# Kernel tuning notes

Hardware: AMD Instinct MI355X
Metric: run time of the kernel (lower is better)

The kernel has to match this reference:

```python
import jax, jax.numpy as jnp
import numpy as np

N_NODES = 100000
N_EDGES = 1600000
G_DIM, H1, H2 = 128, 64, 32
HEADS = 4
NUM_REL = 3
NUM_CLASSES = 7


def setup_inputs() -> dict:
    key = jax.random.key(0)
    ks = jax.random.split(key, 16)
    s = 0.05
    inp = {
        "x": jax.random.normal(ks[0], (N_NODES, G_DIM), dtype=jnp.float32),
        "lengths": N_NODES,
        "edge_index": jax.random.randint(ks[1], (2, N_EDGES), 0, N_NODES),
        "edge_type": jax.random.randint(ks[2], (N_EDGES,), 0, NUM_REL),
        # RGCNConv params (root weight + per-relation weights + bias)
        "W_rel": jax.random.normal(ks[3], (NUM_REL, G_DIM, H1), dtype=jnp.float32) * s,
        "W_root": jax.random.normal(ks[4], (G_DIM, H1), dtype=jnp.float32) * s,
        "b_rgcn": jax.random.normal(ks[5], (H1,), dtype=jnp.float32) * s,
        # TransformerConv params (heads*H2 = 128 output, concat=True default)
        "Wq": jax.random.normal(ks[6], (H1, HEADS * H2), dtype=jnp.float32) * s,
        "bq": jax.random.normal(ks[7], (HEADS * H2,), dtype=jnp.float32) * s,
        "Wk": jax.random.normal(ks[8], (H1, HEADS * H2), dtype=jnp.float32) * s,
        "bk": jax.random.normal(ks[9], (HEADS * H2,), dtype=jnp.float32) * s,
        "Wv": jax.random.normal(ks[10], (H1, HEADS * H2), dtype=jnp.float32) * s,
        "bv": jax.random.normal(ks[11], (HEADS * H2,), dtype=jnp.float32) * s,
        "Wskip": jax.random.normal(ks[12], (H1, HEADS * H2), dtype=jnp.float32) * s,
        "bskip": jax.random.normal(ks[13], (HEADS * H2,), dtype=jnp.float32) * s,
        # final classifier (in = heads*H2 since TransformerConv concat=True)
        "Wf": jax.random.normal(ks[14], (HEADS * H2, NUM_CLASSES), dtype=jnp.float32) * s,
        "bf": jax.random.normal(ks[15], (NUM_CLASSES,), dtype=jnp.float32) * s,
    }
    return inp


def _forward(x, edge_index, edge_type, W_rel, W_root, b_rgcn,
             Wq, bq, Wk, bk, Wv, bv, Wskip, bskip, Wf, bf):
    n = x.shape[0]
    src, dst = edge_index[0], edge_index[1]  # source -> target flow

    # ---- RGCNConv: root transform + per-relation mean aggregation ----
    h = x @ W_root + b_rgcn  # [N, H1]
    for r in range(NUM_REL):
        hr = x @ W_rel[r]  # [N, H1] transform at node level (cheap)
        mask = (edge_type == r)
        msg = jnp.where(mask[:, None], hr[src], 0.0)  # [E, H1]
        ssum = jax.ops.segment_sum(msg, dst, num_segments=n)
        cnt = jax.ops.segment_sum(mask.astype(x.dtype), dst, num_segments=n)
        h = h + jnp.where(cnt[:, None] > 0, ssum / jnp.maximum(cnt, 1.0)[:, None], 0.0)
    h = jax.nn.relu(h)

    # ---- TransformerConv (heads=4, concat=True, root skip) ----
    Q = (h @ Wq + bq).reshape(n, HEADS, H2)
    K = (h @ Wk + bk).reshape(n, HEADS, H2)
    V = (h @ Wv + bv).reshape(n, HEADS, H2)
    scores = jnp.sum(Q[dst] * K[src], axis=-1) / jnp.sqrt(jnp.asarray(H2, x.dtype))  # [E, HEADS]
    smax = jax.ops.segment_max(scores, dst, num_segments=n)  # [N, HEADS]
    e = jnp.exp(scores - smax[dst])
    denom = jax.ops.segment_sum(e, dst, num_segments=n)  # [N, HEADS]
    alpha = e / jnp.maximum(denom[dst], 1e-16)  # [E, HEADS]
    agg = jax.ops.segment_sum(alpha[..., None] * V[src], dst, num_segments=n)  # [N, HEADS, H2]
    out = agg.reshape(n, HEADS * H2) + h @ Wskip + bskip
    out = jax.nn.relu(out)

    return out @ Wf + bf  # [N, NUM_CLASSES]


def reference(x, lengths, edge_index, edge_type, W_rel, W_root, b_rgcn,
              Wq, bq, Wk, bk, Wv, bv, Wskip, bskip, Wf, bf):
    # lengths is accepted but unused by the original forward
    return _forward(x, edge_index, edge_type, W_rel, W_root, b_rgcn,
                    Wq, bq, Wk, bk, Wv, bv, Wskip, bskip, Wf, bf)
```

## Files before the change

### kernel.cpp

```cpp
#include <hip/hip_runtime.h>
#include <math.h>

#define N_NODES 100000
#define N_EDGES 1600000

typedef short short8 __attribute__((ext_vector_type(8)));
typedef float f32x4 __attribute__((ext_vector_type(4)));
typedef float f32x2 __attribute__((ext_vector_type(2)));
typedef _Float16 h2 __attribute__((ext_vector_type(2)));

#define QSC 0.25503540f

static __device__ __forceinline__ float bf2f(unsigned int u16) {
    return __uint_as_float(u16 << 16);
}
static __device__ __forceinline__ unsigned short f2bf(float f) {
    unsigned u = __float_as_uint(f);
    unsigned r = u + 0x7FFF + ((u >> 16) & 1);
    return (unsigned short)(r >> 16);
}
static __device__ __forceinline__ f32x2 bfpair(unsigned u) {
    f32x2 r;
    r.x = __uint_as_float(u << 16);
    r.y = __uint_as_float(u & 0xFFFF0000u);
    return r;
}
static __device__ __forceinline__ float dot8h(const h2* q, uint4 k) {
    h2 s = q[0] * __builtin_bit_cast(h2, k.x);
    s += q[1] * __builtin_bit_cast(h2, k.y);
    s += q[2] * __builtin_bit_cast(h2, k.z);
    s += q[3] * __builtin_bit_cast(h2, k.w);
    return (float)s.x + (float)s.y;
}
static __device__ __forceinline__ void pv8h(h2* o, float w, uint4 v) {
    _Float16 wh = (_Float16)w;
    o[0] += wh * __builtin_bit_cast(h2, v.x);
    o[1] += wh * __builtin_bit_cast(h2, v.y);
    o[2] += wh * __builtin_bit_cast(h2, v.z);
    o[3] += wh * __builtin_bit_cast(h2, v.w);
}

__global__ void repack_kernel(const float* __restrict__ Wrel, const float* __restrict__ Wroot,
                              const float* __restrict__ Wq, const float* __restrict__ Wk,
                              const float* __restrict__ Wv, const float* __restrict__ Wsk,
                              const float* __restrict__ bq, const float* __restrict__ bk,
                              const float* __restrict__ bv, const float* __restrict__ bsk,
                              unsigned short* __restrict__ W1t, unsigned short* __restrict__ W2t,
                              float* __restrict__ bcat) {
    int idx = blockIdx.x * 256 + threadIdx.x;
    if (idx < 128 * 256) {
        int k = idx >> 8, c = idx & 255;
        float v;
        if (c < 192) { int r = c >> 6, cc = c & 63; v = Wrel[r * 8192 + k * 64 + cc]; }
        else v = Wroot[k * 64 + (c - 192)];
        W1t[c * 128 + k] = f2bf(v);
    }
    int i2 = idx - 128 * 256;
    if (i2 >= 0 && i2 < 64 * 512) {
        int k = i2 >> 9, c = i2 & 511;
        float v;
        if (c < 128) v = Wq[k * 128 + c];
        else if (c < 256) v = Wk[k * 128 + c - 128];
        else if (c < 384) v = Wv[k * 128 + c - 256];
        else v = Wsk[k * 128 + c - 384];
        W2t[c * 64 + k] = f2bf(v);
    }
    int i3 = idx - 128 * 256 - 64 * 512;
    if (i3 >= 0 && i3 < 512) {
        float v;
        if (i3 < 128) v = bq[i3];
        else if (i3 < 256) v = bk[i3 - 128];
        else if (i3 < 384) v = bv[i3 - 256];
        else v = bsk[i3 - 384];
        bcat[i3] = v;
    }
}

__global__ void hist_kernel(const int* __restrict__ ei, const int* __restrict__ et,
                            int* __restrict__ cntr, int* __restrict__ rank) {
    int e = blockIdx.x * 256 + threadIdx.x;
    if (e < N_EDGES) rank[e] = atomicAdd(&cntr[et[e] * N_NODES + ei[N_EDGES + e]], 1);
}

__global__ void scanA_kernel(const int* __restrict__ cntr, int* __restrict__ part) {
    __shared__ int wsum[4];
    int t = threadIdx.x;
    int base = blockIdx.x * 1024 + t * 4;
    int s = 0;
    for (int i = 0; i < 4; i++) {
        int idx = base + i;
        if (idx < N_NODES) s += cntr[idx] + cntr[N_NODES + idx] + cntr[2 * N_NODES + idx];
    }
    for (int off = 1; off < 64; off <<= 1) s += __shfl_xor(s, off);
    if ((t & 63) == 0) wsum[t >> 6] = s;
    __syncthreads();
    if (t == 0) part[blockIdx.x] = wsum[0] + wsum[1] + wsum[2] + wsum[3];
}

__global__ void scanC_kernel(const int* __restrict__ cntr, const int* __restrict__ part,
                             uint4* __restrict__ bro) {
    __shared__ int wsum[4];
    __shared__ int ws2[4];
    int t = threadIdx.x;
    int lane = t & 63;
    int base = blockIdx.x * 1024 + t * 4;
    int c0v[4], c1v[4], c2v[4]; int tsum = 0;
    for (int i = 0; i < 4; i++) {
        int idx = base + i;
        if (idx < N_NODES) {
            c0v[i] = cntr[idx]; c1v[i] = cntr[N_NODES + idx]; c2v[i] = cntr[2 * N_NODES + idx];
        } else { c0v[i] = c1v[i] = c2v[i] = 0; }
        tsum += c0v[i] + c1v[i] + c2v[i];
    }
    int p = (t < blockIdx.x) ? part[t] : 0;
    for (int off = 1; off < 64; off <<= 1) p += __shfl_xor(p, off);
    if (lane == 0) ws2[t >> 6] = p;
    int x = tsum;
    for (int off = 1; off < 64; off <<= 1) { int y = __shfl_up(x, off); if (lane >= off) x += y; }
    if (lane == 63) wsum[t >> 6] = x;
    __syncthreads();
    if (t == 0) { int run = 0; for (int w = 0; w < 4; w++) { int tmp = wsum[w]; wsum[w] = run; run += tmp; } }
    __syncthreads();
    int bofs = ws2[0] + ws2[1] + ws2[2] + ws2[3];
    int excl = x - tsum + wsum[t >> 6] + bofs;
    for (int i = 0; i < 4; i++) {
        int idx = base + i;
        if (idx < N_NODES) {
            uint4 b;
            b.x = (unsigned)excl;
            b.y = (unsigned)(excl + c0v[i]);
            b.z = (unsigned)(excl + c0v[i] + c1v[i]);
            b.w = (unsigned)(excl + c0v[i] + c1v[i] + c2v[i]);
            bro[idx] = b;
        }
        excl += c0v[i] + c1v[i] + c2v[i];
    }
}

__global__ void scatter_kernel(const int* __restrict__ ei, const int* __restrict__ et,
                               const uint4* __restrict__ bro, const int* __restrict__ rank,
                               unsigned int* __restrict__ ep) {
    int e = blockIdx.x * 256 + threadIdx.x;
    if (e >= N_EDGES) return;
    int src = ei[e], dst = ei[N_EDGES + e], r = et[e], rk = rank[e];
    uint4 b = bro[dst];
    unsigned ofs = (r == 0) ? b.x : (r == 1) ? b.y : b.z;
    ep[ofs + rk] = ((unsigned)src << 2) | (unsigned)r;
}

__global__ __launch_bounds__(256) void gemm1_mfma(const float* __restrict__ X,
                                                  const unsigned short* __restrict__ W1t,
                                                  unsigned short* __restrict__ hr_all) {
    __shared__ unsigned short As[64][136];
    __shared__ unsigned short Bs[64][136];
    int t = threadIdx.x;
    int rb = blockIdx.x * 64;
    #pragma unroll
    for (int i = 0; i < 8; i++) {
        int lin = t + i * 256;
        int row = lin >> 5;
        int c4 = lin & 31;
        float4 v = make_float4(0.f, 0.f, 0.f, 0.f);
        int gr = rb + row;
        if (gr < N_NODES) v = *(const float4*)&X[gr * 128 + c4 * 4];
        unsigned w0 = (unsigned)f2bf(v.x) | ((unsigned)f2bf(v.y) << 16);
        unsigned w1 = (unsigned)f2bf(v.z) | ((unsigned)f2bf(v.w) << 16);
        *(uint2*)&As[row][c4 * 4] = make_uint2(w0, w1);
    }
    int w = t >> 6, l = t & 63;
    int wr = (w >> 1) * 32, wc = (w & 1) * 32;
    int lr = l & 15, lk = (l >> 4) * 8;
    int drow = (l >> 4) * 4;
    int dcol = l & 15;
    for (int cb4 = 0; cb4 < 4; cb4++) {
        int cb = cb4 * 64;
        __syncthreads();
        #pragma unroll
        for (int i = 0; i < 4; i++) {
            int lin = t + i * 256;
            int n = lin >> 4;
            int k8 = lin & 15;
            *(uint4*)&Bs[n][k8 * 8] = *(const uint4*)&W1t[(cb + n) * 128 + k8 * 8];
        }
        __syncthreads();
        f32x4 c00 = {0.f,0.f,0.f,0.f}, c01 = {0.f,0.f,0.f,0.f};
        f32x4 c10 = {0.f,0.f,0.f,0.f}, c11 = {0.f,0.f,0.f,0.f};
        #pragma unroll
        for (int kk = 0; kk < 128; kk += 32) {
            short8 a0 = *(const short8*)&As[wr + lr][kk + lk];
            short8 a1 = *(const short8*)&As[wr + 16 + lr][kk + lk];
            short8 b0 = *(const short8*)&Bs[wc + lr][kk + lk];
            short8 b1 = *(const short8*)&Bs[wc + 16 + lr][kk + lk];
            c00 = __builtin_amdgcn_mfma_f32_16x16x32_bf16(a0, b0, c00, 0, 0, 0);
            c01 = __builtin_amdgcn_mfma_f32_16x16x32_bf16(a0, b1, c01, 0, 0, 0);
            c10 = __builtin_amdgcn_mfma_f32_16x16x32_bf16(a1, b0, c10, 0, 0, 0);
            c11 = __builtin_amdgcn_mfma_f32_16x16x32_bf16(a1, b1, c11, 0, 0, 0);
        }
        f32x4 cc[2][2] = {{c00, c01}, {c10, c11}};
        #pragma unroll
        for (int i = 0; i < 2; i++)
            #pragma unroll
            for (int j = 0; j < 2; j++)
                #pragma unroll
                for (int rg = 0; rg < 4; rg++) {
                    int gr = rb + wr + i * 16 + drow + rg;
                    int gc = cb + wc + j * 16 + dcol;
                    if (gr < N_NODES) hr_all[gr * 256 + gc] = f2bf(cc[i][j][rg]);
                }
    }
}

__global__ __launch_bounds__(256) void rgcn_kernel(const unsigned short* __restrict__ hr,
                                                   const float* __restrict__ brg,
                                                   const uint4* __restrict__ bro,
                                                   const unsigned int* __restrict__ ep,
                                                   unsigned short* __restrict__ Hm) {
    int t = threadIdx.x, lane = t & 63;
    int n = blockIdx.x * 4 + (t >> 6);
    if (n >= N_NODES) return;
    int slot = lane >> 4, pos = lane & 15;
    const uint2* H2 = (const uint2*)hr;
    uint4 b = bro[n];
    int p0 = (int)b.x, p1 = (int)b.w;
    int c0 = (int)(b.y - b.x), c1 = (int)(b.z - b.y), c2 = (int)(b.w - b.z);
    float i0 = c0 ? 1.f / (float)c0 : 0.f;
    float i1 = c1 ? 1.f / (float)c1 : 0.f;
    float i2 = c2 ? 1.f / (float)c2 : 0.f;
    f32x2 a01 = {0.f, 0.f}, a23 = {0.f, 0.f};
    for (int base = p0; base < p1; base += 64) {
        int pc = base + lane;
        unsigned chunk = (pc < p1) ? ep[pc] : 0u;
        int cnt = min(64, p1 - base);
        int g0 = 0;
        for (; g0 + 16 <= cnt; g0 += 16) {
            int i0x = g0 + slot;
            int e0 = __shfl((int)chunk, i0x);
            int e1 = __shfl((int)chunk, i0x + 4);
            int e2 = __shfl((int)chunk, i0x + 8);
            int e3 = __shfl((int)chunk, i0x + 12);
            float w0 = ((e0 & 3) == 0) ? i0 : ((e0 & 3) == 1) ? i1 : i2;
            float w1 = ((e1 & 3) == 0) ? i0 : ((e1 & 3) == 1) ? i1 : i2;
            float w2 = ((e2 & 3) == 0) ? i0 : ((e2 & 3) == 1) ? i1 : i2;
            float w3 = ((e3 & 3) == 0) ? i0 : ((e3 & 3) == 1) ? i1 : i2;
            uint2 h0 = H2[(unsigned)e0 * 16 + pos];
            uint2 h1 = H2[(unsigned)e1 * 16 + pos];
            uint2 h2v = H2[(unsigned)e2 * 16 + pos];
            uint2 h3 = H2[(unsigned)e3 * 16 + pos];
            a01 += w0 * bfpair(h0.x); a23 += w0 * bfpair(h0.y);
            a01 += w1 * bfpair(h1.x); a23 += w1 * bfpair(h1.y);
            a01 += w2 * bfpair(h2v.x); a23 += w2 * bfpair(h2v.y);
            a01 += w3 * bfpair(h3.x); a23 += w3 * bfpair(h3.y);
        }
        for (; g0 < cnt; g0 += 8) {
            int iA = g0 + slot, iB = iA + 4;
            int e0 = __shfl((int)chunk, iA);
            int e1 = __shfl((int)chunk, iB);
            float w0 = ((e0 & 3) == 0) ? i0 : ((e0 & 3) == 1) ? i1 : i2;
            float w1 = ((e1 & 3) == 0) ? i0 : ((e1 & 3) == 1) ? i1 : i2;
            w0 = (iA < cnt) ? w0 : 0.f;
            w1 = (iB < cnt) ? w1 : 0.f;
            uint2 h0 = H2[(unsigned)e0 * 16 + pos];
            uint2 h1 = H2[(unsigned)e1 * 16 + pos];
            a01 += w0 * bfpair(h0.x); a23 += w0 * bfpair(h0.y);
            a01 += w1 * bfpair(h1.x); a23 += w1 * bfpair(h1.y);
        }
    }
    a01.x += __shfl_xor(a01.x, 16); a01.x += __shfl_xor(a01.x, 32);
    a01.y += __shfl_xor(a01.y, 16); a01.y += __shfl_xor(a01.y, 32);
    a23.x += __shfl_xor(a23.x, 16); a23.x += __shfl_xor(a23.x, 32);
    a23.y += __shfl_xor(a23.y, 16); a23.y += __shfl_xor(a23.y, 32);
    uint2 rt = H2[(n * 4 + 3) * 16 + pos];
    f32x2 r01 = bfpair(rt.x), r23 = bfpair(rt.y);
    float4 bb = ((const float4*)brg)[pos];
    float h0 = fmaxf(r01.x + bb.x + a01.x, 0.f);
    float h1 = fmaxf(r01.y + bb.y + a01.y, 0.f);
    float h2s = fmaxf(r23.x + bb.z + a23.x, 0.f);
    float h3 = fmaxf(r23.y + bb.w + a23.y, 0.f);
    if (slot == 0) {
        uint2 wv;
        wv.x = (unsigned)f2bf(h0) | ((unsigned)f2bf(h1) << 16);
        wv.y = (unsigned)f2bf(h2s) | ((unsigned)f2bf(h3) << 16);
        ((uint2*)Hm)[n * 16 + pos] = wv;
    }
}

__global__ __launch_bounds__(256) void gemm2_mfma(const unsigned short* __restrict__ Hm,
                                                  const unsigned short* __restrict__ W2t,
                                                  const float* __restrict__ bcat,
                                                  _Float16* __restrict__ QS, _Float16* __restrict__ KV) {
    __shared__ unsigned short As[64][72];
    __shared__ unsigned short Bs[64][72];
    int t = threadIdx.x;
    int rb = blockIdx.x * 64;
    #pragma unroll
    for (int i = 0; i < 2; i++) {
        int lin = t + i * 256;
        int row = lin >> 3;
        int k8 = lin & 7;
        uint4 v = make_uint4(0, 0, 0, 0);
        int gr = rb + row;
        if (gr < N_NODES) v = *(const uint4*)&Hm[gr * 64 + k8 * 8];
        *(uint4*)&As[row][k8 * 8] = v;
    }
    int w = t >> 6, l = t & 63;
    int wr = (w >> 1) * 32, wc = (w & 1) * 32;
    int lr = l & 15, lk = (l >> 4) * 8;
    int drow = (l >> 4) * 4;
    int dcol = l & 15;
    for (int cb8 = 0; cb8 < 8; cb8++) {
        int cb = cb8 * 64;
        float qsc = (cb8 < 2) ? QSC : 1.f;
        __syncthreads();
        #pragma unroll
        for (int i = 0; i < 2; i++) {
            int lin = t + i * 256;
            int n = lin >> 3;
            int k8 = lin & 7;
            *(uint4*)&Bs[n][k8 * 8] = *(const uint4*)&W2t[(cb + n) * 64 + k8 * 8];
        }
        __syncthreads();
        f32x4 c00 = {0.f,0.f,0.f,0.f}, c01 = {0.f,0.f,0.f,0.f};
        f32x4 c10 = {0.f,0.f,0.f,0.f}, c11 = {0.f,0.f,0.f,0.f};
        #pragma unroll
        for (int kk = 0; kk < 64; kk += 32) {
            short8 a0 = *(const short8*)&As[wr + lr][kk + lk];
            short8 a1 = *(const short8*)&As[wr + 16 + lr][kk + lk];
            short8 b0 = *(const short8*)&Bs[wc + lr][kk + lk];
            short8 b1 = *(const short8*)&Bs[wc + 16 + lr][kk + lk];
            c00 = __builtin_amdgcn_mfma_f32_16x16x32_bf16(a0, b0, c00, 0, 0, 0);
            c01 = __builtin_amdgcn_mfma_f32_16x16x32_bf16(a0, b1, c01, 0, 0, 0);
            c10 = __builtin_amdgcn_mfma_f32_16x16x32_bf16(a1, b0, c10, 0, 0, 0);
            c11 = __builtin_amdgcn_mfma_f32_16x16x32_bf16(a1, b1, c11, 0, 0, 0);
        }
        f32x4 cc[2][2] = {{c00, c01}, {c10, c11}};
        #pragma unroll
        for (int i = 0; i < 2; i++)
            #pragma unroll
            for (int j = 0; j < 2; j++)
                #pragma unroll
                for (int rg = 0; rg < 4; rg++) {
                    int gr = rb + wr + i * 16 + drow + rg;
                    int gc = cb + wc + j * 16 + dcol;
                    if (gr >= N_NODES) continue;
                    float v = (cc[i][j][rg] + bcat[gc]) * qsc;
                    _Float16 h = (_Float16)v;
                    if (gc < 128) QS[gr * 256 + gc] = h;
                    else if (gc < 384) KV[gr * 256 + gc - 128] = h;
                    else QS[gr * 256 + gc - 256] = h;
                }
    }
}

__global__ __launch_bounds__(256) void attn_kernel(const _Float16* __restrict__ QS,
                                                   const _Float16* __restrict__ KV,
                                                   const uint4* __restrict__ bro,
                                                   const unsigned int* __restrict__ ep,
                                                   const float* __restrict__ Wf, const float* __restrict__ bfv,
                                                   float* __restrict__ out) {
    int t = threadIdx.x, lane = t & 63;
    int n = blockIdx.x * 4 + (t >> 6);
    if (n >= N_NODES) return;
    int slot = lane >> 4, pos = lane & 15;
    const uint4* KV4 = (const uint4*)KV;
    const uint4* QS4 = (const uint4*)QS;
    uint4 qv = QS4[n * 32 + pos];
    h2 qh[4] = { __builtin_bit_cast(h2, qv.x), __builtin_bit_cast(h2, qv.y),
                 __builtin_bit_cast(h2, qv.z), __builtin_bit_cast(h2, qv.w) };
    h2 o[4] = { h2{0,0}, h2{0,0}, h2{0,0}, h2{0,0} };
    float d = 0.f;
    uint4 bnd = bro[n];
    int p0 = (int)bnd.x, p1 = (int)bnd.w;
    for (int base = p0; base < p1; base += 64) {
        int pc = base + lane;
        unsigned chunk = (pc < p1) ? ep[pc] : 0u;
        int cnt = min(64, p1 - base);
        int g0 = 0;
        for (; g0 + 16 <= cnt; g0 += 16) {
            int i0 = g0 + slot;
            int e0 = __shfl((int)chunk, i0);
            int e1 = __shfl((int)chunk, i0 + 4);
            int e2 = __shfl((int)chunk, i0 + 8);
            int e3 = __shfl((int)chunk, i0 + 12);
            int b0 = ((e0 >> 2) << 5) + pos;
            int b1 = ((e1 >> 2) << 5) + pos;
            int b2 = ((e2 >> 2) << 5) + pos;
            int b3 = ((e3 >> 2) << 5) + pos;
            uint4 k0 = KV4[b0], v0 = KV4[b0 + 16];
            uint4 k1 = KV4[b1], v1 = KV4[b1 + 16];
            uint4 k2 = KV4[b2], v2 = KV4[b2 + 16];
            uint4 k3 = KV4[b3], v3 = KV4[b3 + 16];
            float d0 = dot8h(qh, k0);
            float d1 = dot8h(qh, k1);
            float d2 = dot8h(qh, k2);
            float d3 = dot8h(qh, k3);
            d0 += __shfl_xor(d0, 1); d1 += __shfl_xor(d1, 1); d2 += __shfl_xor(d2, 1); d3 += __shfl_xor(d3, 1);
            d0 += __shfl_xor(d0, 2); d1 += __shfl_xor(d1, 2); d2 += __shfl_xor(d2, 2); d3 += __shfl_xor(d3, 2);
            float w0 = __builtin_amdgcn_exp2f(d0);
            float w1 = __builtin_amdgcn_exp2f(d1);
            float w2 = __builtin_amdgcn_exp2f(d2);
            float w3 = __builtin_amdgcn_exp2f(d3);
            d += (w0 + w1) + (w2 + w3);
            pv8h(o, w0, v0); pv8h(o, w1, v1); pv8h(o, w2, v2); pv8h(o, w3, v3);
        }
        for (; g0 < cnt; g0 += 8) {
            int iA = g0 + slot, iB = iA + 4;
            int e0 = __shfl((int)chunk, iA);
            int e1 = __shfl((int)chunk, iB);
            int b0 = ((e0 >> 2) << 5) + pos;
            int b1 = ((e1 >> 2) << 5) + pos;
            uint4 k0 = KV4[b0], v0 = KV4[b0 + 16];
            uint4 k1 = KV4[b1], v1 = KV4[b1 + 16];
            float d0 = dot8h(qh, k0);
            float d1 = dot8h(qh, k1);
            d0 += __shfl_xor(d0, 1); d1 += __shfl_xor(d1, 1);
            d0 += __shfl_xor(d0, 2); d1 += __shfl_xor(d1, 2);
            float w0 = (iA < cnt) ? __builtin_amdgcn_exp2f(d0) : 0.f;
            float w1 = (iB < cnt) ? __builtin_amdgcn_exp2f(d1) : 0.f;
            d += w0 + w1;
            pv8h(o, w0, v0); pv8h(o, w1, v1);
        }
    }
    float of[8];
    #pragma unroll
    for (int i = 0; i < 4; i++) { of[2 * i] = (float)o[i].x; of[2 * i + 1] = (float)o[i].y; }
    d += __shfl_xor(d, 16); d += __shfl_xor(d, 32);
    #pragma unroll
    for (int i = 0; i < 8; i++) { of[i] += __shfl_xor(of[i], 16); of[i] += __shfl_xor(of[i], 32); }
    float inv = (d > 0.f) ? 1.f / d : 0.f;
    uint4 sv = QS4[n * 32 + 16 + pos];
    h2 sh[4] = { __builtin_bit_cast(h2, sv.x), __builtin_bit_cast(h2, sv.y),
                 __builtin_bit_cast(h2, sv.z), __builtin_bit_cast(h2, sv.w) };
    float rf[8];
    #pragma unroll
    for (int i = 0; i < 4; i++) {
        rf[2 * i]     = fmaxf((float)sh[i].x + of[2 * i] * inv, 0.f);
        rf[2 * i + 1] = fmaxf((float)sh[i].y + of[2 * i + 1] * inv, 0.f);
    }
    float rr0 = (slot == 0) ? rf[0] : (slot == 1) ? rf[2] : (slot == 2) ? rf[4] : rf[6];
    float rr1 = (slot == 0) ? rf[1] : (slot == 1) ? rf[3] : (slot == 2) ? rf[5] : rf[7];
    int gd = pos * 8 + slot * 2;
    float acc[7];
    #pragma unroll
    for (int j = 0; j < 7; j++) acc[j] = rr0 * Wf[gd * 7 + j] + rr1 * Wf[gd * 7 + 7 + j];
    #pragma unroll
    for (int j = 0; j < 7; j++) {
        acc[j] += __shfl_xor(acc[j], 1);
        acc[j] += __shfl_xor(acc[j], 2);
        acc[j] += __shfl_xor(acc[j], 4);
        acc[j] += __shfl_xor(acc[j], 8);
        acc[j] += __shfl_xor(acc[j], 16);
        acc[j] += __shfl_xor(acc[j], 32);
    }
    if (lane == 0) {
        #pragma unroll
        for (int j = 0; j < 7; j++) out[n * 7 + j] = acc[j] + bfv[j];
    }
}

extern "C" void kernel_launch(void* const* d_in, const int* in_sizes, int n_in,
                              void* d_out, int out_size, void* d_ws, size_t ws_size,
                              hipStream_t stream) {
    const float* x     = (const float*)d_in[0];
    const int*   ei    = (const int*)d_in[2];
    const int*   et    = (const int*)d_in[3];
    const float* Wrel  = (const float*)d_in[4];
    const float* Wroot = (const float*)d_in[5];
    const float* brg   = (const float*)d_in[6];
    const float* Wq    = (const float*)d_in[7];
    const float* bq    = (const float*)d_in[8];
    const float* Wk    = (const float*)d_in[9];
    const float* bk    = (const float*)d_in[10];
    const float* Wv    = (const float*)d_in[11];
    const float* bv    = (const float*)d_in[12];
    const float* Wsk   = (const float*)d_in[13];
    const float* bsk   = (const float*)d_in[14];
    const float* Wf    = (const float*)d_in[15];
    const float* bfv   = (const float*)d_in[16];
    float* out = (float*)d_out;

    char* ws = (char*)d_ws;
    unsigned short* hr_all = (unsigned short*)(ws + 0);
    _Float16*       QS     = (_Float16*)(ws + 0);
    _Float16*       KV     = (_Float16*)(ws + 51200000);
    unsigned short* Hm     = (unsigned short*)(ws + 102400000);
    unsigned int*   ep     = (unsigned int*)(ws + 115200000);
    int*            rank   = (int*)(ws + 121600000);
    uint4*          bro    = (uint4*)(ws + 128000000);
    int*            cntr   = (int*)(ws + 129600016);
    int*            part   = (int*)(ws + 130800016);
    unsigned short* W1t    = (unsigned short*)(ws + 130800528);
    unsigned short* W2t    = (unsigned short*)(ws + 130866064);
    float*          bcat   = (float*)(ws + 130931600);

    hipMemsetAsync(cntr, 0, 3 * N_NODES * sizeof(int), stream);

    repack_kernel<<<258, 256, 0, stream>>>(Wrel, Wroot, Wq, Wk, Wv, Wsk, bq, bk, bv, bsk, W1t, W2t, bcat);

    hist_kernel<<<N_EDGES / 256, 256, 0, stream>>>(ei, et, cntr, rank);
    scanA_kernel<<<98, 256, 0, stream>>>(cntr, part);
    scanC_kernel<<<98, 256, 0, stream>>>(cntr, part, bro);
    scatter_kernel<<<N_EDGES / 256, 256, 0, stream>>>(ei, et, bro, rank, ep);

    gemm1_mfma<<<1563, 256, 0, stream>>>(x, W1t, hr_all);
    rgcn_kernel<<<25000, 256, 0, stream>>>(hr_all, brg, bro, ep, Hm);

    gemm2_mfma<<<1563, 256, 0, stream>>>(Hm, W2t, bcat, QS, KV);
    attn_kernel<<<25000, 256, 0, stream>>>(QS, KV, bro, ep, Wf, bfv, out);
}
```

Baseline: 440.1 us.

## Store K/V in FP8, simplify edge loops, pack relation into rank

K and V are stored as FP8 (when the conversion builtins exist), halving the gather traffic in the attention kernel, and accumulation moves to fp32. The shuffle-based chunked edge loops in the RGCN and attention kernels become direct per-slot ep loads. The relation type is packed into the rank word so the scatter kernel skips reading edge_type. The classifier epilogue is also restructured to use fewer shuffles. FP8 K/V lowers accuracy and may exceed tolerance.

```diff
diff --git a/kernel.cpp b/kernel.cpp
--- a/kernel.cpp
+++ b/kernel.cpp
@@ -10,6 +10,15 @@
 typedef _Float16 h2 __attribute__((ext_vector_type(2)));
 
 #define QSC 0.25503540f
+
+#if defined(__has_builtin)
+#if __has_builtin(__builtin_amdgcn_cvt_pk_f32_fp8) && __has_builtin(__builtin_amdgcn_cvt_pk_fp8_f32)
+#define HAVE_FP8 1
+#endif
+#endif
+#ifndef HAVE_FP8
+#define HAVE_FP8 0
+#endif
 
 static __device__ __forceinline__ float bf2f(unsigned int u16) {
     return __uint_as_float(u16 << 16);
@@ -24,20 +33,6 @@
     r.x = __uint_as_float(u << 16);
     r.y = __uint_as_float(u & 0xFFFF0000u);
     return r;
-}
-static __device__ __forceinline__ float dot8h(const h2* q, uint4 k) {
-    h2 s = q[0] * __builtin_bit_cast(h2, k.x);
-    s += q[1] * __builtin_bit_cast(h2, k.y);
-    s += q[2] * __builtin_bit_cast(h2, k.z);
-    s += q[3] * __builtin_bit_cast(h2, k.w);
-    return (float)s.x + (float)s.y;
-}
-static __device__ __forceinline__ void pv8h(h2* o, float w, uint4 v) {
-    _Float16 wh = (_Float16)w;
-    o[0] += wh * __builtin_bit_cast(h2, v.x);
-    o[1] += wh * __builtin_bit_cast(h2, v.y);
-    o[2] += wh * __builtin_bit_cast(h2, v.z);
-    o[3] += wh * __builtin_bit_cast(h2, v.w);
 }
 
 __global__ void repack_kernel(const float* __restrict__ Wrel, const float* __restrict__ Wroot,
@@ -77,9 +72,13 @@
 }
 
 __global__ void hist_kernel(const int* __restrict__ ei, const int* __restrict__ et,
-                            int* __restrict__ cntr, int* __restrict__ rank) {
+                            int* __restrict__ cntr, unsigned* __restrict__ rank) {
     int e = blockIdx.x * 256 + threadIdx.x;
-    if (e < N_EDGES) rank[e] = atomicAdd(&cntr[et[e] * N_NODES + ei[N_EDGES + e]], 1);
+    if (e < N_EDGES) {
+        int r = et[e];
+        unsigned rk = (unsigned)atomicAdd(&cntr[r * N_NODES + ei[N_EDGES + e]], 1);
+        rank[e] = rk | ((unsigned)r << 28);
+    }
 }
 
 __global__ void scanA_kernel(const int* __restrict__ cntr, int* __restrict__ part) {
@@ -137,12 +136,15 @@
     }
 }
 
-__global__ void scatter_kernel(const int* __restrict__ ei, const int* __restrict__ et,
-                               const uint4* __restrict__ bro, const int* __restrict__ rank,
+__global__ void scatter_kernel(const int* __restrict__ ei,
+                               const uint4* __restrict__ bro, const unsigned* __restrict__ rank,
                                unsigned int* __restrict__ ep) {
     int e = blockIdx.x * 256 + threadIdx.x;
     if (e >= N_EDGES) return;
-    int src = ei[e], dst = ei[N_EDGES + e], r = et[e], rk = rank[e];
+    int src = ei[e], dst = ei[N_EDGES + e];
+    unsigned rkr = rank[e];
+    int r = (int)(rkr >> 28);
+    unsigned rk = rkr & 0x0FFFFFFFu;
     uint4 b = bro[dst];
     unsigned ofs = (r == 0) ? b.x : (r == 1) ? b.y : b.z;
     ep[ofs + rk] = ((unsigned)src << 2) | (unsigned)r;
@@ -227,43 +229,29 @@
     float i1 = c1 ? 1.f / (float)c1 : 0.f;
     float i2 = c2 ? 1.f / (float)c2 : 0.f;
     f32x2 a01 = {0.f, 0.f}, a23 = {0.f, 0.f};
-    for (int base = p0; base < p1; base += 64) {
-        int pc = base + lane;
-        unsigned chunk = (pc < p1) ? ep[pc] : 0u;
-        int cnt = min(64, p1 - base);
-        int g0 = 0;
-        for (; g0 + 16 <= cnt; g0 += 16) {
-            int i0x = g0 + slot;
-            int e0 = __shfl((int)chunk, i0x);
-            int e1 = __shfl((int)chunk, i0x + 4);
-            int e2 = __shfl((int)chunk, i0x + 8);
-            int e3 = __shfl((int)chunk, i0x + 12);
-            float w0 = ((e0 & 3) == 0) ? i0 : ((e0 & 3) == 1) ? i1 : i2;
-            float w1 = ((e1 & 3) == 0) ? i0 : ((e1 & 3) == 1) ? i1 : i2;
-            float w2 = ((e2 & 3) == 0) ? i0 : ((e2 & 3) == 1) ? i1 : i2;
-            float w3 = ((e3 & 3) == 0) ? i0 : ((e3 & 3) == 1) ? i1 : i2;
-            uint2 h0 = H2[(unsigned)e0 * 16 + pos];
-            uint2 h1 = H2[(unsigned)e1 * 16 + pos];
-            uint2 h2v = H2[(unsigned)e2 * 16 + pos];
-            uint2 h3 = H2[(unsigned)e3 * 16 + pos];
-            a01 += w0 * bfpair(h0.x); a23 += w0 * bfpair(h0.y);
-            a01 += w1 * bfpair(h1.x); a23 += w1 * bfpair(h1.y);
-            a01 += w2 * bfpair(h2v.x); a23 += w2 * bfpair(h2v.y);
-            a01 += w3 * bfpair(h3.x); a23 += w3 * bfpair(h3.y);
-        }
-        for (; g0 < cnt; g0 += 8) {
-            int iA = g0 + slot, iB = iA + 4;
-            int e0 = __shfl((int)chunk, iA);
-            int e1 = __shfl((int)chunk, iB);
-            float w0 = ((e0 & 3) == 0) ? i0 : ((e0 & 3) == 1) ? i1 : i2;
-            float w1 = ((e1 & 3) == 0) ? i0 : ((e1 & 3) == 1) ? i1 : i2;
-            w0 = (iA < cnt) ? w0 : 0.f;
-            w1 = (iB < cnt) ? w1 : 0.f;
-            uint2 h0 = H2[(unsigned)e0 * 16 + pos];
-            uint2 h1 = H2[(unsigned)e1 * 16 + pos];
-            a01 += w0 * bfpair(h0.x); a23 += w0 * bfpair(h0.y);
-            a01 += w1 * bfpair(h1.x); a23 += w1 * bfpair(h1.y);
-        }
+    int idx = p0 + slot;
+    while (idx + 12 < p1) {
+        unsigned e0 = ep[idx], e1 = ep[idx + 4], e2 = ep[idx + 8], e3 = ep[idx + 12];
+        uint2 h0 = H2[e0 * 16 + pos];
+        uint2 h1 = H2[e1 * 16 + pos];
+        uint2 h2v = H2[e2 * 16 + pos];
+        uint2 h3 = H2[e3 * 16 + pos];
+        float w0 = ((e0 & 3) == 0) ? i0 : ((e0 & 3) == 1) ? i1 : i2;
+        float w1 = ((e1 & 3) == 0) ? i0 : ((e1 & 3) == 1) ? i1 : i2;
+        float w2 = ((e2 & 3) == 0) ? i0 : ((e2 & 3) == 1) ? i1 : i2;
+        float w3 = ((e3 & 3) == 0) ? i0 : ((e3 & 3) == 1) ? i1 : i2;
+        a01 += w0 * bfpair(h0.x); a23 += w0 * bfpair(h0.y);
+        a01 += w1 * bfpair(h1.x); a23 += w1 * bfpair(h1.y);
+        a01 += w2 * bfpair(h2v.x); a23 += w2 * bfpair(h2v.y);
+        a01 += w3 * bfpair(h3.x); a23 += w3 * bfpair(h3.y);
+        idx += 16;
+    }
+    while (idx < p1) {
+        unsigned e0 = ep[idx];
+        uint2 h0 = H2[e0 * 16 + pos];
+        float w0 = ((e0 & 3) == 0) ? i0 : ((e0 & 3) == 1) ? i1 : i2;
+        a01 += w0 * bfpair(h0.x); a23 += w0 * bfpair(h0.y);
+        idx += 4;
     }
     a01.x += __shfl_xor(a01.x, 16); a01.x += __shfl_xor(a01.x, 32);
     a01.y += __shfl_xor(a01.y, 16); a01.y += __shfl_xor(a01.y, 32);
@@ -287,7 +275,12 @@
 __global__ __launch_bounds__(256) void gemm2_mfma(const unsigned short* __restrict__ Hm,
                                                   const unsigned short* __restrict__ W2t,
                                                   const float* __restrict__ bcat,
-                                                  _Float16* __restrict__ QS, _Float16* __restrict__ KV) {
+                                                  _Float16* __restrict__ QS, void* __restrict__ KVp) {
+#if HAVE_FP8
+    unsigned char* KV = (unsigned char*)KVp;
+#else
+    _Float16* KV = (_Float16*)KVp;
+#endif
     __shared__ unsigned short As[64][72];
     __shared__ unsigned short Bs[64][72];
     int t = threadIdx.x;
@@ -343,16 +336,63 @@
                     int gc = cb + wc + j * 16 + dcol;
                     if (gr >= N_NODES) continue;
                     float v = (cc[i][j][rg] + bcat[gc]) * qsc;
-                    _Float16 h = (_Float16)v;
-                    if (gc < 128) QS[gr * 256 + gc] = h;
-                    else if (gc < 384) KV[gr * 256 + gc - 128] = h;
-                    else QS[gr * 256 + gc - 256] = h;
+                    if (gc < 128) QS[gr * 256 + gc] = (_Float16)v;
+                    else if (gc < 384) {
+#if HAVE_FP8
+                        unsigned pk = (unsigned)__builtin_amdgcn_cvt_pk_fp8_f32(v, v, 0, false);
+                        KV[gr * 256 + gc - 128] = (unsigned char)(pk & 0xFF);
+#else
+                        KV[gr * 256 + gc - 128] = (_Float16)v;
+#endif
+                    }
+                    else QS[gr * 256 + gc - 256] = (_Float16)v;
                 }
     }
 }
 
+#if HAVE_FP8
+static __device__ __forceinline__ void attn_edge(const f32x2* qf, uint2 ku, uint2 vu,
+                                                 f32x2& o01, f32x2& o23, f32x2& o45, f32x2& o67,
+                                                 float& d) {
+    f32x2 k01 = __builtin_amdgcn_cvt_pk_f32_fp8(ku.x, false);
+    f32x2 k23 = __builtin_amdgcn_cvt_pk_f32_fp8(ku.x, true);
+    f32x2 k45 = __builtin_amdgcn_cvt_pk_f32_fp8(ku.y, false);
+    f32x2 k67 = __builtin_amdgcn_cvt_pk_f32_fp8(ku.y, true);
+    f32x2 s2 = qf[0] * k01 + qf[1] * k23 + qf[2] * k45 + qf[3] * k67;
+    float s = s2.x + s2.y;
+    s += __shfl_xor(s, 1);
+    s += __shfl_xor(s, 2);
+    float w = __builtin_amdgcn_exp2f(s);
+    d += w;
+    o01 += w * __builtin_amdgcn_cvt_pk_f32_fp8(vu.x, false);
+    o23 += w * __builtin_amdgcn_cvt_pk_f32_fp8(vu.x, true);
+    o45 += w * __builtin_amdgcn_cvt_pk_f32_fp8(vu.y, false);
+    o67 += w * __builtin_amdgcn_cvt_pk_f32_fp8(vu.y, true);
+}
+#else
+static __device__ __forceinline__ void attn_edge16(const f32x2* qf, uint4 ku, uint4 vu,
+                                                   f32x2& o01, f32x2& o23, f32x2& o45, f32x2& o67,
+                                                   float& d) {
+    h2 k0 = __builtin_bit_cast(h2, ku.x), k1 = __builtin_bit_cast(h2, ku.y);
+    h2 k2 = __builtin_bit_cast(h2, ku.z), k3 = __builtin_bit_cast(h2, ku.w);
+    f32x2 s2 = qf[0] * f32x2{(float)k0.x, (float)k0.y} + qf[1] * f32x2{(float)k1.x, (float)k1.y}
+             + qf[2] * f32x2{(float)k2.x, (float)k2.y} + qf[3] * f32x2{(float)k3.x, (float)k3.y};
+    float s = s2.x + s2.y;
+    s += __shfl_xor(s, 1);
+    s += __shfl_xor(s, 2);
+    float w = __builtin_amdgcn_exp2f(s);
+    d += w;
+    h2 v0 = __builtin_bit_cast(h2, vu.x), v1 = __builtin_bit_cast(h2, vu.y);
+    h2 v2 = __builtin_bit_cast(h2, vu.z), v3 = __builtin_bit_cast(h2, vu.w);
+    o01 += w * f32x2{(float)v0.x, (float)v0.y};
+    o23 += w * f32x2{(float)v1.x, (float)v1.y};
+    o45 += w * f32x2{(float)v2.x, (float)v2.y};
+    o67 += w * f32x2{(float)v3.x, (float)v3.y};
+}
+#endif
+
 __global__ __launch_bounds__(256) void attn_kernel(const _Float16* __restrict__ QS,
-                                                   const _Float16* __restrict__ KV,
+                                                   const void* __restrict__ KVp,
                                                    const uint4* __restrict__ bro,
                                                    const unsigned int* __restrict__ ep,
                                                    const float* __restrict__ Wf, const float* __restrict__ bfv,
@@ -361,99 +401,96 @@
     int n = blockIdx.x * 4 + (t >> 6);
     if (n >= N_NODES) return;
     int slot = lane >> 4, pos = lane & 15;
-    const uint4* KV4 = (const uint4*)KV;
     const uint4* QS4 = (const uint4*)QS;
     uint4 qv = QS4[n * 32 + pos];
-    h2 qh[4] = { __builtin_bit_cast(h2, qv.x), __builtin_bit_cast(h2, qv.y),
-                 __builtin_bit_cast(h2, qv.z), __builtin_bit_cast(h2, qv.w) };
-    h2 o[4] = { h2{0,0}, h2{0,0}, h2{0,0}, h2{0,0} };
+    h2 q0 = __builtin_bit_cast(h2, qv.x), q1 = __builtin_bit_cast(h2, qv.y);
+    h2 q2 = __builtin_bit_cast(h2, qv.z), q3 = __builtin_bit_cast(h2, qv.w);
+    f32x2 qf[4] = { f32x2{(float)q0.x, (float)q0.y}, f32x2{(float)q1.x, (float)q1.y},
+                    f32x2{(float)q2.x, (float)q2.y}, f32x2{(float)q3.x, (float)q3.y} };
+    f32x2 o01 = {0.f,0.f}, o23 = {0.f,0.f}, o45 = {0.f,0.f}, o67 = {0.f,0.f};
     float d = 0.f;
     uint4 bnd = bro[n];
     int p0 = (int)bnd.x, p1 = (int)bnd.w;
-    for (int base = p0; base < p1; base += 64) {
-        int pc = base + lane;
-        unsigned chunk = (pc < p1) ? ep[pc] : 0u;
-        int cnt = min(64, p1 - base);
-        int g0 = 0;
-        for (; g0 + 16 <= cnt; g0 += 16) {
-            int i0 = g0 + slot;
-            int e0 = __shfl((int)chunk, i0);
-            int e1 = __shfl((int)chunk, i0 + 4);
-            int e2 = __shfl((int)chunk, i0 + 8);
-            int e3 = __shfl((int)chunk, i0 + 12);
-            int b0 = ((e0 >> 2) << 5) + pos;
-            int b1 = ((e1 >> 2) << 5) + pos;
-            int b2 = ((e2 >> 2) << 5) + pos;
-            int b3 = ((e3 >> 2) << 5) + pos;
-            uint4 k0 = KV4[b0], v0 = KV4[b0 + 16];
-            uint4 k1 = KV4[b1], v1 = KV4[b1 + 16];
-            uint4 k2 = KV4[b2], v2 = KV4[b2 + 16];
-            uint4 k3 = KV4[b3], v3 = KV4[b3 + 16];
-            float d0 = dot8h(qh, k0);
-            float d1 = dot8h(qh, k1);
-            float d2 = dot8h(qh, k2);
-            float d3 = dot8h(qh, k3);
-            d0 += __shfl_xor(d0, 1); d1 += __shfl_xor(d1, 1); d2 += __shfl_xor(d2, 1); d3 += __shfl_xor(d3, 1);
-            d0 += __shfl_xor(d0, 2); d1 += __shfl_xor(d1, 2); d2 += __shfl_xor(d2, 2); d3 += __shfl_xor(d3, 2);
-            float w0 = __builtin_amdgcn_exp2f(d0);
-            float w1 = __builtin_amdgcn_exp2f(d1);
-            float w2 = __builtin_amdgcn_exp2f(d2);
-            float w3 = __builtin_amdgcn_exp2f(d3);
-            d += (w0 + w1) + (w2 + w3);
-            pv8h(o, w0, v0); pv8h(o, w1, v1); pv8h(o, w2, v2); pv8h(o, w3, v3);
-        }
-        for (; g0 < cnt; g0 += 8) {
-            int iA = g0 + slot, iB = iA + 4;
-            int e0 = __shfl((int)chunk, iA);
-            int e1 = __shfl((int)chunk, iB);
-            int b0 = ((e0 >> 2) << 5) + pos;
-            int b1 = ((e1 >> 2) << 5) + pos;
-            uint4 k0 = KV4[b0], v0 = KV4[b0 + 16];
-            uint4 k1 = KV4[b1], v1 = KV4[b1 + 16];
-            float d0 = dot8h(qh, k0);
-            float d1 = dot8h(qh, k1);
-            d0 += __shfl_xor(d0, 1); d1 += __shfl_xor(d1, 1);
-            d0 += __shfl_xor(d0, 2); d1 += __shfl_xor(d1, 2);
-            float w0 = (iA < cnt) ? __builtin_amdgcn_exp2f(d0) : 0.f;
-            float w1 = (iB < cnt) ? __builtin_amdgcn_exp2f(d1) : 0.f;
-            d += w0 + w1;
-            pv8h(o, w0, v0); pv8h(o, w1, v1);
-        }
-    }
-    float of[8];
-    #pragma unroll
-    for (int i = 0; i < 4; i++) { of[2 * i] = (float)o[i].x; of[2 * i + 1] = (float)o[i].y; }
+    int idx = p0 + slot;
+#if HAVE_FP8
+    const uint2* KV2 = (const uint2*)KVp;
+    while (idx + 12 < p1) {
+        unsigned e0 = ep[idx], e1 = ep[idx + 4], e2 = ep[idx + 8], e3 = ep[idx + 12];
+        int b0 = (int)(e0 >> 2) * 32 + pos;
+        int b1 = (int)(e1 >> 2) * 32 + pos;
+        int b2 = (int)(e2 >> 2) * 32 + pos;
+        int b3 = (int)(e3 >> 2) * 32 + pos;
+        uint2 k0 = KV2[b0], v0 = KV2[b0 + 16];
+        uint2 k1 = KV2[b1], v1 = KV2[b1 + 16];
+        uint2 k2 = KV2[b2], v2 = KV2[b2 + 16];
+        uint2 k3 = KV2[b3], v3 = KV2[b3 + 16];
+        attn_edge(qf, k0, v0, o01, o23, o45, o67, d);
+        attn_edge(qf, k1, v1, o01, o23, o45, o67, d);
+        attn_edge(qf, k2, v2, o01, o23, o45, o67, d);
+        attn_edge(qf, k3, v3, o01, o23, o45, o67, d);
+        idx += 16;
+    }
+    while (idx < p1) {
+        unsigned e0 = ep[idx];
+        int b0 = (int)(e0 >> 2) * 32 + pos;
+        uint2 k0 = KV2[b0], v0 = KV2[b0 + 16];
+        attn_edge(qf, k0, v0, o01, o23, o45, o67, d);
+        idx += 4;
+    }
+#else
+    const uint4* KV4 = (const uint4*)KVp;
+    while (idx + 12 < p1) {
+        unsigned e0 = ep[idx], e1 = ep[idx + 4], e2 = ep[idx + 8], e3 = ep[idx + 12];
+        int b0 = (int)(e0 >> 2) * 32 + pos;
+        int b1 = (int)(e1 >> 2) * 32 + pos;
+        int b2 = (int)(e2 >> 2) * 32 + pos;
+        int b3 = (int)(e3 >> 2) * 32 + pos;
+        uint4 k0 = KV4[b0], v0 = KV4[b0 + 16];
+        uint4 k1 = KV4[b1], v1 = KV4[b1 + 16];
+        uint4 k2 = KV4[b2], v2 = KV4[b2 + 16];
+        uint4 k3 = KV4[b3], v3 = KV4[b3 + 16];
+        attn_edge16(qf, k0, v0, o01, o23, o45, o67, d);
+        attn_edge16(qf, k1, v1, o01, o23, o45, o67, d);
+        attn_edge16(qf, k2, v2, o01, o23, o45, o67, d);
+        attn_edge16(qf, k3, v3, o01, o23, o45, o67, d);
+        idx += 16;
+    }
+    while (idx < p1) {
+        unsigned e0 = ep[idx];
+        int b0 = (int)(e0 >> 2) * 32 + pos;
+        uint4 k0 = KV4[b0], v0 = KV4[b0 + 16];
+        attn_edge16(qf, k0, v0, o01, o23, o45, o67, d);
+        idx += 4;
+    }
+#endif
+    float of[8] = { o01.x, o01.y, o23.x, o23.y, o45.x, o45.y, o67.x, o67.y };
     d += __shfl_xor(d, 16); d += __shfl_xor(d, 32);
     #pragma unroll
     for (int i = 0; i < 8; i++) { of[i] += __shfl_xor(of[i], 16); of[i] += __shfl_xor(of[i], 32); }
     float inv = (d > 0.f) ? 1.f / d : 0.f;
     uint4 sv = QS4[n * 32 + 16 + pos];
-    h2 sh[4] = { __builtin_bit_cast(h2, sv.x), __builtin_bit_cast(h2, sv.y),
-                 __builtin_bit_cast(h2, sv.z), __builtin_bit_cast(h2, sv.w) };
+    h2 s0 = __builtin_bit_cast(h2, sv.x), s1 = __builtin_bit_cast(h2, sv.y);
+    h2 s2 = __builtin_bit_cast(h2, sv.z), s3 = __builtin_bit_cast(h2, sv.w);
+    float sf[8] = { (float)s0.x, (float)s0.y, (float)s1.x, (float)s1.y,
+                    (float)s2.x, (float)s2.y, (float)s3.x, (float)s3.y };
     float rf[8];
     #pragma unroll
-    for (int i = 0; i < 4; i++) {
-        rf[2 * i]     = fmaxf((float)sh[i].x + of[2 * i] * inv, 0.f);
-        rf[2 * i + 1] = fmaxf((float)sh[i].y + of[2 * i + 1] * inv, 0.f);
-    }
-    float rr0 = (slot == 0) ? rf[0] : (slot == 1) ? rf[2] : (slot == 2) ? rf[4] : rf[6];
-    float rr1 = (slot == 0) ? rf[1] : (slot == 1) ? rf[3] : (slot == 2) ? rf[5] : rf[7];
-    int gd = pos * 8 + slot * 2;
-    float acc[7];
+    for (int i = 0; i < 8; i++) rf[i] = fmaxf(sf[i] + of[i] * inv, 0.f);
+    int base_d = pos * 8;
+    int cls1 = (slot < 3) ? slot + 4 : 0;
+    float a0 = 0.f, a1 = 0.f;
     #pragma unroll
-    for (int j = 0; j < 7; j++) acc[j] = rr0 * Wf[gd * 7 + j] + rr1 * Wf[gd * 7 + 7 + j];
-    #pragma unroll
-    for (int j = 0; j < 7; j++) {
-        acc[j] += __shfl_xor(acc[j], 1);
-        acc[j] += __shfl_xor(acc[j], 2);
-        acc[j] += __shfl_xor(acc[j], 4);
-        acc[j] += __shfl_xor(acc[j], 8);
-        acc[j] += __shfl_xor(acc[j], 16);
-        acc[j] += __shfl_xor(acc[j], 32);
-    }
-    if (lane == 0) {
-        #pragma unroll
-        for (int j = 0; j < 7; j++) out[n * 7 + j] = acc[j] + bfv[j];
+    for (int i = 0; i < 8; i++) {
+        a0 += rf[i] * Wf[(base_d + i) * 7 + slot];
+        a1 += rf[i] * Wf[(base_d + i) * 7 + cls1];
+    }
+    a0 += __shfl_xor(a0, 1); a1 += __shfl_xor(a1, 1);
+    a0 += __shfl_xor(a0, 2); a1 += __shfl_xor(a1, 2);
+    a0 += __shfl_xor(a0, 4); a1 += __shfl_xor(a1, 4);
+    a0 += __shfl_xor(a0, 8); a1 += __shfl_xor(a1, 8);
+    if (pos == 0) {
+        out[n * 7 + slot] = a0 + bfv[slot];
+        if (slot < 3) out[n * 7 + slot + 4] = a1 + bfv[slot + 4];
     }
 }
 
@@ -481,10 +518,10 @@
     char* ws = (char*)d_ws;
     unsigned short* hr_all = (unsigned short*)(ws + 0);
     _Float16*       QS     = (_Float16*)(ws + 0);
-    _Float16*       KV     = (_Float16*)(ws + 51200000);
+    void*           KV     = (void*)(ws + 51200000);
     unsigned short* Hm     = (unsigned short*)(ws + 102400000);
     unsigned int*   ep     = (unsigned int*)(ws + 115200000);
-    int*            rank   = (int*)(ws + 121600000);
+    unsigned*       rank   = (unsigned*)(ws + 121600000);
     uint4*          bro    = (uint4*)(ws + 128000000);
     int*            cntr   = (int*)(ws + 129600016);
     int*            part   = (int*)(ws + 130800016);
@@ -499,7 +536,7 @@
     hist_kernel<<<N_EDGES / 256, 256, 0, stream>>>(ei, et, cntr, rank);
     scanA_kernel<<<98, 256, 0, stream>>>(cntr, part);
     scanC_kernel<<<98, 256, 0, stream>>>(cntr, part, bro);
-    scatter_kernel<<<N_EDGES / 256, 256, 0, stream>>>(ei, et, bro, rank, ep);
+    scatter_kernel<<<N_EDGES / 256, 256, 0, stream>>>(ei, bro, rank, ep);
 
     gemm1_mfma<<<1563, 256, 0, stream>>>(x, W1t, hr_all);
     rgcn_kernel<<<25000, 256, 0, stream>>>(hr_all, brg, bro, ep, Hm);
```

Measured after the change: 573.8 us. 1.3x slower.
